# Optimization experiments

Hardware: AMD Instinct MI355X
Metric: run time of the kernel (lower is better)

The kernel has to match this reference:

```python
import jax, jax.numpy as jnp
import numpy as np

B, T = 64, 2048
HID, FAST, SLOW, VOCAB = 256, 64, 256, 64
WRITE_THRESH = 0.4
NEG = -1000000000.0


def setup_inputs() -> dict:
    key = jax.random.key(0)
    ks = jax.random.split(key, 10)
    s = 0.05  # small init so gate sigmoids are not saturated
    return {
        "seq": jax.random.randint(ks[0], (B, T), 0, VOCAB),
        "emb": jax.random.normal(ks[1], (VOCAB, HID), jnp.float32),        # encoder embedding table
        "Wg": jax.random.normal(ks[2], (HID, 1), jnp.float32) * s,         # write_gate
        "bg": jnp.zeros((1,), jnp.float32),
        "Wd": jax.random.normal(ks[3], (HID, 1), jnp.float32) * s,         # demotion_net
        "bd": jnp.zeros((1,), jnp.float32),
        "Wq": jax.random.normal(ks[4], (HID, HID), jnp.float32) * s,       # read_head.q_proj
        "bq": jnp.zeros((HID,), jnp.float32),
        "Wo": jax.random.normal(ks[5], (HID, VOCAB), jnp.float32) * s,     # read_head.out
        "bo": jnp.zeros((VOCAB,), jnp.float32),
    }


def _process_sequence(h, Wg, bg, Wd, bd):
    # h: (B, T, H). Sequential LRU tiered-memory scatter, vectorized over batch.
    Bb, Tt, H = h.shape

    def step(state, tok_h):
        fm, sm, fa, sa, fu, su = state
        ws = jax.nn.sigmoid(tok_h @ Wg + bg)[:, 0]          # (B,) write score
        act = ws >= WRITE_THRESH                            # skip rows with score < 0.4
        fa = fa + fu.astype(jnp.int32)                      # age occupied slots
        sa = sa + su.astype(jnp.int32)
        free = ~fu
        has_free = jnp.any(free, axis=1)                    # (B,)
        free_idx = jnp.argmax(free, axis=1)                 # first free fast slot
        dem = ((fm @ Wd)[..., 0] + bd[0])                   # (B, FAST) demotion scores
        dem_slot = jnp.argmin(dem, axis=1)
        fslot = jnp.where(has_free, free_idx, dem_slot)     # fast slot to write
        foh = jax.nn.one_hot(fslot, FAST, dtype=bool)
        wf = act[:, None] & foh                              # (B, FAST) fast-write mask
        # value demoted to slow (only used when fast was full)
        demoted = jnp.take_along_axis(fm, fslot[:, None, None], axis=1)[:, 0, :]
        slow_act = act & ~has_free
        sfree = ~su
        s_has_free = jnp.any(sfree, axis=1)
        ss = jnp.where(s_has_free, jnp.argmax(sfree, axis=1), jnp.argmax(sa, axis=1))
        soh = jax.nn.one_hot(ss, SLOW, dtype=bool)
        wsm = slow_act[:, None] & soh                        # (B, SLOW) slow-write mask
        sm = jnp.where(wsm[..., None], demoted[:, None, :], sm)
        sa = jnp.where(wsm, 0, sa)
        su = su | wsm
        tok = jax.lax.stop_gradient(tok_h)                   # original writes tok_h.detach()
        fm = jnp.where(wf[..., None], tok[:, None, :], fm)
        fa = jnp.where(wf, 0, fa)
        fu = fu | wf
        return (fm, sm, fa, sa, fu, su), None

    init = (
        jnp.zeros((Bb, FAST, H), h.dtype),
        jnp.zeros((Bb, SLOW, H), h.dtype),
        jnp.zeros((Bb, FAST), jnp.int32),
        jnp.zeros((Bb, SLOW), jnp.int32),
        jnp.zeros((Bb, FAST), bool),
        jnp.zeros((Bb, SLOW), bool),
    )
    hs = jnp.swapaxes(h[:, : Tt - 3], 0, 1)                  # loop runs for T-3 tokens
    (fm, sm, fa, sa, fu, su), _ = jax.lax.scan(step, init, hs)
    memory = jnp.concatenate([fm, sm], axis=1)               # (B, F+S, H)
    mask = jnp.concatenate([fu, su], axis=1).astype(h.dtype)
    slow_mask = su.astype(h.dtype)
    return memory, mask, slow_mask


def reference(seq, emb, Wg, bg, Wd, bd, Wq, bq, Wo, bo):
    h = emb[seq]                                             # encoder: (B, T, H)
    memory, mask, slow_mask = _process_sequence(h, Wg, bg, Wd, bd)
    # ReadHead
    q = h[:, -1, :] @ Wq + bq                                # (B, H)
    scores = jnp.einsum("bnh,bh->bn", memory, q)
    scores = jnp.where(mask == 0, NEG, scores)
    attn = jax.nn.softmax(scores, axis=-1)
    ctx = jnp.einsum("bn,bnh->bh", attn, memory)
    logits = ctx @ Wo + bo                                   # (B, VOCAB)
    return logits, slow_mask
```

## Files before the change

kernel.cpp:

```cpp
#include <hip/hip_runtime.h>
#include <math.h>

#define BB 64
#define TT 2048
#define HIDD 256
#define FASTN 64
#define SLOWN 256
#define VOC 64
#define TLOOP (TT - 3)
#define NEGC -1000000000.0f
#define EPAD 257
#define NEGBIG (-(1 << 20))
#define BYTEAT(U, J) ((int)(((U) >> (8 * (J))) & 0xFFu))

__global__ __launch_bounds__(512) void k_one(
    const int* __restrict__ seq, const float* __restrict__ emb,
    const float* __restrict__ Wg, const float* __restrict__ bg,
    const float* __restrict__ Wd, const float* __restrict__ bd,
    const float* __restrict__ Wq, const float* __restrict__ bq,
    const float* __restrict__ Wo, const float* __restrict__ bo,
    float* __restrict__ out) {
  const int b = blockIdx.x;
  const int tid = threadIdx.x;
  const int lane = tid & 63;
  const int wv = tid >> 6;

  __shared__ float embS[VOC * EPAD];
  __shared__ float WoS[HIDD * VOC];
  __shared__ __align__(16) unsigned char zsB[2304];
  __shared__ float qLastS[HIDD], ctxS[HIDD];
  __shared__ float pp[4][64];
  __shared__ float gp8[8][64], dp8[8][64];
  __shared__ float wS[64];
  __shared__ int prS[64], invS[64], cntTok[64];
  __shared__ int CS[4];
  __shared__ int PsS[8][64], QsS[8][64], aEndS[8][64], eSS[8][64];

  const int4* seq4 = (const int4*)(seq + b * TT);
  int4 sqa = make_int4(0, 0, 0, 0), sqb = make_int4(0, 0, 0, 0);
  if (tid < 256) { sqa = seq4[2 * tid]; sqb = seq4[2 * tid + 1]; }
  const int lastv = seq[b * TT + TT - 1];

  const float4* emb4 = (const float4*)emb;
  for (int i = tid; i < VOC * 64; i += 512) {
    float4 e = emb4[i];
    float* d = &embS[(i >> 6) * EPAD + ((i & 63) << 2)];
    d[0] = e.x; d[1] = e.y; d[2] = e.z; d[3] = e.w;
  }
  {
    const float4* Wo4 = (const float4*)Wo;
    float4* WoS4 = (float4*)WoS;
    for (int i = tid; i < HIDD * VOC / 4; i += 512) WoS4[i] = Wo4[i];
  }
  __syncthreads();

  {
    const int v = tid & 63, kp = tid >> 6;
    const float* er = &embS[v * EPAD + kp * 32];
    const float* wg = &Wg[kp * 32];
    const float* wd = &Wd[kp * 32];
    float g = 0.f, d = 0.f;
#pragma unroll 8
    for (int k = 0; k < 32; ++k) { float e = er[k]; g += e * wg[k]; d += e * wd[k]; }
    gp8[kp][v] = g; dp8[kp][v] = d;
  }
  __syncthreads();

  float qacc = 0.f;
  if (tid < 64) {
    float g = bg[0], dv = bd[0];
#pragma unroll
    for (int p = 0; p < 8; ++p) { g += gp8[p][tid]; dv += dp8[p][tid]; }
    int act = (1.f / (1.f + expf(-g)) >= 0.4f) ? 1 : 0;
    int r = 0;
#pragma unroll
    for (int s = 1; s < 64; ++s) {
      float du = __shfl_xor(dv, s);
      int u = lane ^ s;
      r += (du < dv || (du == dv && u < lane)) ? 1 : 0;
    }
    invS[r] = tid;
    prS[tid] = act ? r : 0xFF;
  } else if (tid >= 256) {
    const int j = tid - 256;
    const float* eL = &embS[lastv * EPAD];
#pragma unroll 8
    for (int k = 0; k < 128; ++k) qacc += eL[k] * Wq[k * HIDD + j];
  }
  __syncthreads();

  int by[8], cAct = 0, incl = 0;
  if (tid < 256) {
    const int t0 = tid * 8;
    int tk[8] = {sqa.x, sqa.y, sqa.z, sqa.w, sqb.x, sqb.y, sqb.z, sqb.w};
#pragma unroll
    for (int j = 0; j < 8; ++j) {
      int r = prS[tk[j]];
      by[j] = (t0 + j < TLOOP) ? r : 0xFF;
      cAct += (by[j] != 0xFF) ? 1 : 0;
    }
    incl = cAct;
    for (int s = 1; s < 64; s <<= 1) {
      int t = __shfl_up(incl, s);
      if (lane >= s) incl += t;
    }
    if (lane == 63) CS[wv] = incl;
  } else {
    const int j = tid - 256;
    const float* eL = &embS[lastv * EPAD];
#pragma unroll 8
    for (int k = 128; k < 256; ++k) qacc += eL[k] * Wq[k * HIDD + j];
    qLastS[j] = qacc + bq[j];
  }
  __syncthreads();

  const int A = CS[0] + CS[1] + CS[2] + CS[3];
  const int fsplit = A < 64 ? A : 64;
  const int nL = A - fsplit;
  const int win = nL < 256 ? nL : 256;
  const int wstart = A - win;
  const int L = (((A + 7) >> 3) + 15) & ~15;

  if (tid < 256) {
    int Ow = 0;
#pragma unroll
    for (int w2 = 0; w2 < 4; ++w2) Ow += (w2 < wv) ? CS[w2] : 0;
    int pos = Ow + incl - cAct;
#pragma unroll
    for (int j = 0; j < 8; ++j)
      if (by[j] != 0xFF) zsB[pos++] = (unsigned char)by[j];
  } else {
    const int j = tid - 256;
    out[BB * VOC + b * SLOWN + j] = (j < win) ? 1.0f : 0.0f;
  }
  __syncthreads();

  const int baseW = wv * L;
  const int endW = min(baseW + L, A);

  {
    int P = 0, Q = NEGBIG;
    uint4 cur = *(const uint4*)(zsB + baseW);
    for (int g = baseW; g < endW; g += 16) {
      uint4 nxt = *(const uint4*)(zsB + g + 16);
      unsigned dsw[4] = {cur.x, cur.y, cur.z, cur.w};
      const int gHi = min(g + 16, endW);
      if (gHi == g + 16 && gHi <= fsplit) {
#pragma unroll
        for (int d = 0; d < 4; ++d)
#pragma unroll
          for (int j = 0; j < 4; ++j) {
            int x = (BYTEAT(dsw[d], j) <= lane) ? 1 : 0;
            P += x; Q += x;
          }
      } else if (gHi == g + 16 && g >= fsplit) {
#pragma unroll
        for (int d = 0; d < 4; ++d)
#pragma unroll
          for (int j = 0; j < 4; ++j) {
            int x = (BYTEAT(dsw[d], j) <= lane) ? 1 : 0;
            P += x - 1;
            Q = max(Q + x - 1, x);
          }
      } else {
#pragma unroll
        for (int d = 0; d < 4; ++d)
#pragma unroll
          for (int j = 0; j < 4; ++j) {
            int i = g + d * 4 + j;
            int x = (BYTEAT(dsw[d], j) <= lane) ? 1 : 0;
            bool vld = i < endW;
            bool fil = i < fsplit;
            int p = fil ? x : x - 1;
            int q = fil ? NEGBIG : x;
            int Pn = P + p;
            int Qn = max(Q + p, q);
            P = vld ? Pn : P;
            Q = vld ? Qn : Q;
          }
      }
      cur = nxt;
    }
    PsS[wv][lane] = P;
    QsS[wv][lane] = Q;
  }
  __syncthreads();

  {
    int a = 0;
    for (int w2 = 0; w2 < wv; ++w2)
      a = max(a + PsS[w2][lane], QsS[w2][lane]);
    int e = 0;
    uint4 cur = *(const uint4*)(zsB + baseW);
    for (int g = baseW; g < endW; g += 16) {
      uint4 nxt = *(const uint4*)(zsB + g + 16);
      unsigned dsw[4] = {cur.x, cur.y, cur.z, cur.w};
      const int gHi = min(g + 16, endW);
      const bool full = (gHi == g + 16);
      if (full && gHi <= fsplit) {
#pragma unroll
        for (int d = 0; d < 4; ++d)
#pragma unroll
          for (int j = 0; j < 4; ++j)
            a += (BYTEAT(dsw[d], j) <= lane) ? 1 : 0;
      } else if (full && g >= fsplit && gHi <= wstart) {
#pragma unroll
        for (int d = 0; d < 4; ++d)
#pragma unroll
          for (int j = 0; j < 4; ++j) {
            int xm1 = (BYTEAT(dsw[d], j) <= lane) ? 0 : -1;
            a = max(a, 1) + xm1;
          }
      } else if (full && g >= wstart) {
#pragma unroll
        for (int d = 0; d < 4; ++d)
#pragma unroll
          for (int j = 0; j < 4; ++j) {
            int xm1 = (BYTEAT(dsw[d], j) <= lane) ? 0 : -1;
            e += (a > 0) ? 1 : 0;
            a = max(a, 1) + xm1;
          }
      } else {
#pragma unroll
        for (int d = 0; d < 4; ++d)
#pragma unroll
          for (int j = 0; j < 4; ++j) {
            int i = g + d * 4 + j;
            int x = (BYTEAT(dsw[d], j) <= lane) ? 1 : 0;
            bool vld = i < endW;
            bool fil = i < fsplit;
            bool wg = vld && (i >= wstart);
            e += (wg && a > 0) ? 1 : 0;
            int af = a + x;
            int al = max(a, 1) + (x - 1);
            int an = fil ? af : al;
            a = vld ? an : a;
          }
      }
      cur = nxt;
    }
    aEndS[wv][lane] = a;
    eSS[wv][lane] = e;
  }
  __syncthreads();

  if (tid < 256) {
    const int v = tid & 63, part = tid >> 6;
    const float* er = &embS[v * EPAD + part * 64];
    const float* qr = &qLastS[part * 64];
    float s = 0.f;
#pragma unroll 8
    for (int k = 0; k < 64; ++k) s += er[k] * qr[k];
    pp[part][v] = s;
  }
  __syncthreads();

  if (tid < 64) {
    int af = aEndS[7][lane];
    int et = 0;
#pragma unroll
    for (int w2 = 0; w2 < 8; ++w2) et += eSS[w2][lane];
    int ap = __shfl_up(af, 1); if (lane == 0) ap = 0;
    int ep = __shfl_up(et, 1); if (lane == 0) ep = 0;
    cntTok[invS[lane]] = (af - ap) + (et - ep);
    float sc = pp[0][tid] + pp[1][tid] + pp[2][tid] + pp[3][tid];
    int cc = cntTok[tid];
    float m = (cc > 0) ? sc : NEGC;
    for (int off = 32; off; off >>= 1) m = fmaxf(m, __shfl_xor(m, off));
    float w = (cc > 0) ? (float)cc * expf(sc - m) : 0.f;
    float z = w;
    for (int off = 32; off; off >>= 1) z += __shfl_xor(z, off);
    z += (float)(FASTN + SLOWN - (fsplit + win)) * expf(NEGC - m);
    wS[tid] = w / z;
  }
  __syncthreads();

  if (tid < 256) {
    float cacc = 0.f;
#pragma unroll 8
    for (int u = 0; u < 64; ++u) cacc += wS[u] * embS[u * EPAD + tid];
    ctxS[tid] = cacc;
  }
  __syncthreads();

  if (tid < 256) {
    const int o = tid & 63, part = tid >> 6;
    const float* cr = &ctxS[part * 64];
    const float* wr = &WoS[part * 64 * VOC + o];
    float s = 0.f;
#pragma unroll 8
    for (int k = 0; k < 64; ++k) s += cr[k] * wr[k * VOC];
    pp[part][o] = s;
  }
  __syncthreads();
  if (tid < 64)
    out[b * VOC + tid] = pp[0][tid] + pp[1][tid] + pp[2][tid] + pp[3][tid] + bo[tid];
}

extern "C" void kernel_launch(void* const* d_in, const int* in_sizes, int n_in,
                              void* d_out, int out_size, void* d_ws, size_t ws_size,
                              hipStream_t stream) {
  const int*   seq = (const int*)d_in[0];
  const float* emb = (const float*)d_in[1];
  const float* Wg  = (const float*)d_in[2];
  const float* bg  = (const float*)d_in[3];
  const float* Wd  = (const float*)d_in[4];
  const float* bd  = (const float*)d_in[5];
  const float* Wq  = (const float*)d_in[6];
  const float* bq  = (const float*)d_in[7];
  const float* Wo  = (const float*)d_in[8];
  const float* bo  = (const float*)d_in[9];
  float* out = (float*)d_out;

  k_one<<<dim3(64), dim3(512), 0, stream>>>(seq, emb, Wg, bg, Wd, bd,
                                            Wq, bq, Wo, bo, out);
}
```

Measured before the change: 98.60 us.

## Split fused kernel into scan and read kernels with per-token query precompute

Splits the single fused per-batch kernel into two launches. The first kernel adds 128 extra blocks that compute q for every vocabulary token into workspace, and the scan blocks now drop the large emb/Wo shared-memory staging and read emb straight from global memory. The second kernel does the attention readout per batch, using the precomputed per-token counts and q looked up by the last token. This removes the large LDS footprint and the serial q projection from the scan blocks, at the cost of an extra launch and a round trip through global memory.

```diff
diff --git a/kernel.cpp b/kernel.cpp
--- a/kernel.cpp
+++ b/kernel.cpp
@@ -13,50 +13,54 @@
 #define NEGBIG (-(1 << 20))
 #define BYTEAT(U, J) ((int)(((U) >> (8 * (J))) & 0xFFu))
 
-__global__ __launch_bounds__(512) void k_one(
+__global__ __launch_bounds__(512) void k_scan(
     const int* __restrict__ seq, const float* __restrict__ emb,
     const float* __restrict__ Wg, const float* __restrict__ bg,
     const float* __restrict__ Wd, const float* __restrict__ bd,
     const float* __restrict__ Wq, const float* __restrict__ bq,
-    const float* __restrict__ Wo, const float* __restrict__ bo,
+    float* __restrict__ qTok, int* __restrict__ cntA, int* __restrict__ AA,
     float* __restrict__ out) {
-  const int b = blockIdx.x;
   const int tid = threadIdx.x;
   const int lane = tid & 63;
   const int wv = tid >> 6;
 
-  __shared__ float embS[VOC * EPAD];
-  __shared__ float WoS[HIDD * VOC];
+  if (blockIdx.x >= 64) {
+    const int idx = (int)blockIdx.x - 64;
+    const int u = idx >> 1, h = idx & 1;
+    __shared__ float eS[HIDD];
+    __shared__ float qp[4][128];
+    if (tid < 256) eS[tid] = emb[u * HIDD + tid];
+    __syncthreads();
+    const int jl = tid & 127;
+    const int j = jl + h * 128;
+    const int kp = tid >> 7;
+    const float* e = &eS[kp * 64];
+    const float* w = &Wq[(kp * 64) * HIDD + j];
+    float acc = 0.f;
+#pragma unroll 8
+    for (int k = 0; k < 64; ++k) acc += e[k] * w[k * HIDD];
+    qp[kp][jl] = acc;
+    __syncthreads();
+    if (tid < 128)
+      qTok[u * HIDD + tid + h * 128] =
+          qp[0][tid] + qp[1][tid] + qp[2][tid] + qp[3][tid] + bq[tid + h * 128];
+    return;
+  }
+
+  const int b = blockIdx.x;
   __shared__ __align__(16) unsigned char zsB[2304];
-  __shared__ float qLastS[HIDD], ctxS[HIDD];
-  __shared__ float pp[4][64];
   __shared__ float gp8[8][64], dp8[8][64];
-  __shared__ float wS[64];
-  __shared__ int prS[64], invS[64], cntTok[64];
+  __shared__ int prS[64], invS[64];
   __shared__ int CS[4];
   __shared__ int PsS[8][64], QsS[8][64], aEndS[8][64], eSS[8][64];
 
   const int4* seq4 = (const int4*)(seq + b * TT);
   int4 sqa = make_int4(0, 0, 0, 0), sqb = make_int4(0, 0, 0, 0);
   if (tid < 256) { sqa = seq4[2 * tid]; sqb = seq4[2 * tid + 1]; }
-  const int lastv = seq[b * TT + TT - 1];
-
-  const float4* emb4 = (const float4*)emb;
-  for (int i = tid; i < VOC * 64; i += 512) {
-    float4 e = emb4[i];
-    float* d = &embS[(i >> 6) * EPAD + ((i & 63) << 2)];
-    d[0] = e.x; d[1] = e.y; d[2] = e.z; d[3] = e.w;
-  }
-  {
-    const float4* Wo4 = (const float4*)Wo;
-    float4* WoS4 = (float4*)WoS;
-    for (int i = tid; i < HIDD * VOC / 4; i += 512) WoS4[i] = Wo4[i];
-  }
-  __syncthreads();
 
   {
     const int v = tid & 63, kp = tid >> 6;
-    const float* er = &embS[v * EPAD + kp * 32];
+    const float* er = &emb[v * HIDD + kp * 32];
     const float* wg = &Wg[kp * 32];
     const float* wd = &Wd[kp * 32];
     float g = 0.f, d = 0.f;
@@ -66,7 +70,6 @@
   }
   __syncthreads();
 
-  float qacc = 0.f;
   if (tid < 64) {
     float g = bg[0], dv = bd[0];
 #pragma unroll
@@ -76,16 +79,11 @@
 #pragma unroll
     for (int s = 1; s < 64; ++s) {
       float du = __shfl_xor(dv, s);
-      int u = lane ^ s;
-      r += (du < dv || (du == dv && u < lane)) ? 1 : 0;
+      int u2 = lane ^ s;
+      r += (du < dv || (du == dv && u2 < lane)) ? 1 : 0;
     }
     invS[r] = tid;
     prS[tid] = act ? r : 0xFF;
-  } else if (tid >= 256) {
-    const int j = tid - 256;
-    const float* eL = &embS[lastv * EPAD];
-#pragma unroll 8
-    for (int k = 0; k < 128; ++k) qacc += eL[k] * Wq[k * HIDD + j];
   }
   __syncthreads();
 
@@ -105,12 +103,6 @@
       if (lane >= s) incl += t;
     }
     if (lane == 63) CS[wv] = incl;
-  } else {
-    const int j = tid - 256;
-    const float* eL = &embS[lastv * EPAD];
-#pragma unroll 8
-    for (int k = 128; k < 256; ++k) qacc += eL[k] * Wq[k * HIDD + j];
-    qLastS[j] = qacc + bq[j];
   }
   __syncthreads();
 
@@ -244,7 +236,42 @@
   }
   __syncthreads();
 
-  if (tid < 256) {
+  if (tid < 64) {
+    int af = aEndS[7][lane];
+    int et = 0;
+#pragma unroll
+    for (int w2 = 0; w2 < 8; ++w2) et += eSS[w2][lane];
+    int ap = __shfl_up(af, 1); if (lane == 0) ap = 0;
+    int ep = __shfl_up(et, 1); if (lane == 0) ep = 0;
+    cntA[b * VOC + invS[lane]] = (af - ap) + (et - ep);
+    if (lane == 0) AA[b] = A;
+  }
+}
+
+__global__ __launch_bounds__(256) void k_read(
+    const int* __restrict__ seq, const float* __restrict__ emb,
+    const float* __restrict__ Wo, const float* __restrict__ bo,
+    const float* __restrict__ qTok, const int* __restrict__ cntA,
+    const int* __restrict__ AA, float* __restrict__ out) {
+  const int b = blockIdx.x;
+  const int tid = threadIdx.x;
+
+  __shared__ float embS[VOC * EPAD];
+  __shared__ float qLastS[HIDD], ctxS[HIDD];
+  __shared__ float pp[4][64];
+  __shared__ float wS[64];
+
+  const int lastv = seq[b * TT + TT - 1];
+  qLastS[tid] = qTok[lastv * HIDD + tid];
+  const float4* emb4 = (const float4*)emb;
+  for (int i = tid; i < VOC * 64; i += 256) {
+    float4 e = emb4[i];
+    float* d = &embS[(i >> 6) * EPAD + ((i & 63) << 2)];
+    d[0] = e.x; d[1] = e.y; d[2] = e.z; d[3] = e.w;
+  }
+  __syncthreads();
+
+  {
     const int v = tid & 63, part = tid >> 6;
     const float* er = &embS[v * EPAD + part * 64];
     const float* qr = &qLastS[part * 64];
@@ -256,15 +283,12 @@
   __syncthreads();
 
   if (tid < 64) {
-    int af = aEndS[7][lane];
-    int et = 0;
-#pragma unroll
-    for (int w2 = 0; w2 < 8; ++w2) et += eSS[w2][lane];
-    int ap = __shfl_up(af, 1); if (lane == 0) ap = 0;
-    int ep = __shfl_up(et, 1); if (lane == 0) ep = 0;
-    cntTok[invS[lane]] = (af - ap) + (et - ep);
+    const int A = AA[b];
+    const int fsplit = A < 64 ? A : 64;
+    const int nL = A - fsplit;
+    const int win = nL < 256 ? nL : 256;
     float sc = pp[0][tid] + pp[1][tid] + pp[2][tid] + pp[3][tid];
-    int cc = cntTok[tid];
+    int cc = cntA[b * VOC + tid];
     float m = (cc > 0) ? sc : NEGC;
     for (int off = 32; off; off >>= 1) m = fmaxf(m, __shfl_xor(m, off));
     float w = (cc > 0) ? (float)cc * expf(sc - m) : 0.f;
@@ -275,7 +299,7 @@
   }
   __syncthreads();
 
-  if (tid < 256) {
+  {
     float cacc = 0.f;
 #pragma unroll 8
     for (int u = 0; u < 64; ++u) cacc += wS[u] * embS[u * EPAD + tid];
@@ -283,10 +307,10 @@
   }
   __syncthreads();
 
-  if (tid < 256) {
+  {
     const int o = tid & 63, part = tid >> 6;
     const float* cr = &ctxS[part * 64];
-    const float* wr = &WoS[part * 64 * VOC + o];
+    const float* wr = &Wo[part * 64 * VOC + o];
     float s = 0.f;
 #pragma unroll 8
     for (int k = 0; k < 64; ++k) s += cr[k] * wr[k * VOC];
@@ -312,6 +336,13 @@
   const float* bo  = (const float*)d_in[9];
   float* out = (float*)d_out;
 
-  k_one<<<dim3(64), dim3(512), 0, stream>>>(seq, emb, Wg, bg, Wd, bd,
-                                            Wq, bq, Wo, bo, out);
+  char* ws = (char*)d_ws;
+  float* qTok = (float*)ws;
+  int*   cntA = (int*)(ws + 65536);
+  int*   AA   = (int*)(ws + 65536 + 16384);
+
+  k_scan<<<dim3(192), dim3(512), 0, stream>>>(seq, emb, Wg, bg, Wd, bd,
+                                              Wq, bq, qTok, cntA, AA, out);
+  k_read<<<dim3(64), dim3(256), 0, stream>>>(seq, emb, Wo, bo,
+                                             qTok, cntA, AA, out);
 }
```

After: 95.80 us. -2.8%, faster.
